# Kernel tuning notes

Measured on AMD Instinct MI355X. Metric: run time of the kernel, lower is better.

The kernel has to match this reference:

```python
import jax, jax.numpy as jnp
import numpy as np

NF = 64      # num_feat
NFR = 5      # num_frames
G = 8        # offset/deformable groups
CENTER = NFR // 2
K = 9        # 3x3 taps


def conv3x3(x, w, b):
    y = jax.lax.conv_general_dilated(x, w, (1, 1), 'SAME',
                                     dimension_numbers=('NCHW', 'OIHW', 'NCHW'))
    return y + b[None, :, None, None]


def mdcn(x, offsets, masks, w, b):
    # x: [B,C,H,W]; offsets: [B,2*G*K,H,W] (layout g,k,(y,x)); masks: [B,G*K,H,W]
    B, C, H, W = x.shape
    Cg = C // G
    off = offsets.reshape(B, G, K, 2, H, W)
    oy, ox = off[:, :, :, 0], off[:, :, :, 1]          # [B,G,K,H,W]
    m = masks.reshape(B, G, K, H, W)
    ky = jnp.repeat(jnp.arange(3), 3) - 1              # [K]
    kx = jnp.tile(jnp.arange(3), 3) - 1
    base_y = (ky[:, None, None] + jnp.arange(H)[None, :, None]).astype(x.dtype)  # [K,H,1]
    base_x = (kx[:, None, None] + jnp.arange(W)[None, None, :]).astype(x.dtype)  # [K,1,W]
    py = oy + base_y[None, None]                        # [B,G,K,H,W]
    px = ox + base_x[None, None]
    y0f = jnp.floor(py); x0f = jnp.floor(px)
    ty = py - y0f; tx = px - x0f
    y0 = y0f.astype(jnp.int32); x0 = x0f.astype(jnp.int32)
    xg = x.reshape(B, G, Cg, H * W)

    def gather(yi, xi):
        valid = (yi >= 0) & (yi < H) & (xi >= 0) & (xi < W)
        yc = jnp.clip(yi, 0, H - 1); xc = jnp.clip(xi, 0, W - 1)
        idx = (yc * W + xc).reshape(B, G, 1, K * H * W)
        idx = jnp.broadcast_to(idx, (B, G, Cg, K * H * W))
        v = jnp.take_along_axis(xg, idx, axis=3).reshape(B, G, Cg, K, H, W)
        return v * valid.reshape(B, G, 1, K, H, W)

    v00 = gather(y0, x0); v01 = gather(y0, x0 + 1)
    v10 = gather(y0 + 1, x0); v11 = gather(y0 + 1, x0 + 1)
    ty_ = ty[:, :, None]; tx_ = tx[:, :, None]          # [B,G,1,K,H,W]
    samp = (v00 * (1 - ty_) * (1 - tx_) + v01 * (1 - ty_) * tx_ +
            v10 * ty_ * (1 - tx_) + v11 * ty_ * tx_)
    samp = samp * m[:, :, None]                          # modulation
    wr = w.reshape(-1, G, Cg, K)                         # [Cout,G,Cg,K]
    out = jnp.einsum('bgckhw,ogck->bohw', samp, wr)
    return out + b[None, :, None, None]


def setup_inputs():
    key = jax.random.key(0)
    ks = jax.random.split(key, 16)
    def mk(k, shape, fan_in):
        return jax.random.normal(k, shape, jnp.float32) * (1.0 / np.sqrt(fan_in))
    B, H, W = 1, 160, 160
    return {
        'x':   jax.random.normal(ks[0], (B, NFR, 4, H, W), jnp.float32),
        'fw1': mk(ks[1], (NF, 4, 3, 3), 4 * 9),   'fb1': jnp.zeros((NF,), jnp.float32),
        'fw2': mk(ks[2], (NF, NF, 3, 3), NF * 9), 'fb2': jnp.zeros((NF,), jnp.float32),
        'fw3': mk(ks[3], (NF, NF, 3, 3), NF * 9), 'fb3': jnp.zeros((NF,), jnp.float32),
        'ow1': mk(ks[4], (NF, 2 * NF, 3, 3), 2 * NF * 9), 'ob1': jnp.zeros((NF,), jnp.float32),
        'ow2': mk(ks[5], (NF, NF, 3, 3), NF * 9),         'ob2': jnp.zeros((NF,), jnp.float32),
        'ow3': mk(ks[6], (G * 27, NF, 3, 3), NF * 9) * 0.1,
        'ob3': jnp.zeros((G * 27,), jnp.float32),
        'dw':  mk(ks[7], (NF, NF, 3, 3), NF * 9), 'db': jnp.zeros((NF,), jnp.float32),
    }


def reference(x, fw1, fb1, fw2, fb2, fw3, fb3, ow1, ob1, ow2, ob2, ow3, ob3, dw, db):
    B, N, C, H, W = x.shape
    f = x.reshape(B * N, C, H, W)
    f = jax.nn.relu(conv3x3(f, fw1, fb1))
    f = jax.nn.relu(conv3x3(f, fw2, fb2))
    f = jax.nn.relu(conv3x3(f, fw3, fb3))
    feats = f.reshape(B, N, NF, H, W)
    ref = feats[:, CENTER]                               # [B,NF,H,W]
    nc = np.array([i for i in range(N) if i != CENTER])
    curr = feats[:, nc].reshape(B * (N - 1), NF, H, W)
    ref_t = jnp.broadcast_to(ref[:, None], (B, N - 1, NF, H, W)).reshape(B * (N - 1), NF, H, W)
    cat = jnp.concatenate([ref_t, curr], axis=1)         # [B(N-1),2*NF,H,W]
    o = jax.nn.relu(conv3x3(cat, ow1, ob1))
    o = jax.nn.relu(conv3x3(o, ow2, ob2))
    raw = conv3x3(o, ow3, ob3)                           # [B(N-1),27G,H,W]
    offsets = raw[:, :G * 18]
    masks = jax.nn.sigmoid(raw[:, G * 18:])
    aligned = mdcn(curr, offsets, masks, dw, db)
    aligned = aligned.reshape(B, N - 1, NF, H, W)
    return jnp.concatenate([aligned[:, :CENTER], ref[:, None], aligned[:, CENTER:]], axis=1)
```

## Files before the change

### kernel.cpp

```cpp
#include <hip/hip_runtime.h>
#include <hip/hip_bf16.h>
#include <math.h>

#define HH 160
#define WW 160
#define HWsz (HH*WW)

typedef short bf16x8 __attribute__((ext_vector_type(8)));
typedef float f32x4  __attribute__((ext_vector_type(4)));

__device__ inline ushort f2bf(float f) {
    unsigned int u = __float_as_uint(f);
    unsigned int r = (u + 0x7FFFu + ((u >> 16) & 1u)) >> 16;
    return (ushort)r;
}

__device__ inline void unpk8(uint4 u, float* f) {
    f[0] = __uint_as_float(u.x << 16); f[1] = __uint_as_float(u.x & 0xFFFF0000u);
    f[2] = __uint_as_float(u.y << 16); f[3] = __uint_as_float(u.y & 0xFFFF0000u);
    f[4] = __uint_as_float(u.z << 16); f[5] = __uint_as_float(u.z & 0xFFFF0000u);
    f[6] = __uint_as_float(u.w << 16); f[7] = __uint_as_float(u.w & 0xFFFF0000u);
}

__global__ __launch_bounds__(256)
void pack_all(const float* __restrict__ fw2, const float* __restrict__ fw3,
              const float* __restrict__ ow1, const float* __restrict__ ow2,
              const float* __restrict__ ow3, const float* __restrict__ dw,
              ushort* __restrict__ w2p, ushort* __restrict__ w3p,
              ushort* __restrict__ o1p, ushort* __restrict__ o2p,
              ushort* __restrict__ o3p, ushort* __restrict__ wmp)
{
    const int seg = blockIdx.y;
    const int idx = blockIdx.x * 256 + threadIdx.x;

    if (seg == 5) {
        if (idx >= 18 * 4 * 64) return;
        const int lane = idx & 63;
        const int mt   = (idx >> 6) & 3;
        const int chunk = idx >> 8;
        const int o  = mt * 16 + (lane & 15);
        const int gk = chunk * 4 + (lane >> 4);
        const int g  = gk / 9, k = gk % 9;
        ushort v[8];
#pragma unroll
        for (int j = 0; j < 8; ++j)
            v[j] = f2bf(dw[((size_t)o * 64 + g * 8 + j) * 9 + k]);
        uint4 pk;
        pk.x = (unsigned)v[0] | ((unsigned)v[1] << 16);
        pk.y = (unsigned)v[2] | ((unsigned)v[3] << 16);
        pk.z = (unsigned)v[4] | ((unsigned)v[5] << 16);
        pk.w = (unsigned)v[6] | ((unsigned)v[7] << 16);
        *(uint4*)(wmp + (size_t)idx * 8) = pk;
        return;
    }

    const float* w; ushort* wp; int Cout, Cin, MT_TOT, CIC;
    switch (seg) {
        case 0: w = fw2; wp = w2p; Cout = 64;  Cin = 64;  MT_TOT = 4;  CIC = 2; break;
        case 1: w = fw3; wp = w3p; Cout = 64;  Cin = 64;  MT_TOT = 4;  CIC = 2; break;
        case 2: w = ow1; wp = o1p; Cout = 64;  Cin = 128; MT_TOT = 4;  CIC = 4; break;
        case 3: w = ow2; wp = o2p; Cout = 64;  Cin = 64;  MT_TOT = 4;  CIC = 2; break;
        default: w = ow3; wp = o3p; Cout = 216; Cin = 64; MT_TOT = 16; CIC = 2; break;
    }
    const int total = 9 * CIC * MT_TOT * 64;
    if (idx >= total) return;
    const int lane = idx & 63;
    int t = idx >> 6;
    const int mt  = t % MT_TOT; t /= MT_TOT;
    const int cic = t % CIC;    t /= CIC;
    const int tap = t;
    const int co  = mt * 16 + (lane & 15);
    const int ci0 = cic * 32 + (lane >> 4) * 8;
    ushort v[8];
#pragma unroll
    for (int j = 0; j < 8; ++j) {
        const int ci = ci0 + j;
        float f = 0.f;
        if (co < Cout && ci < Cin) f = w[((size_t)co * Cin + ci) * 9 + tap];
        v[j] = f2bf(f);
    }
    uint4 pk;
    pk.x = (unsigned)v[0] | ((unsigned)v[1] << 16);
    pk.y = (unsigned)v[2] | ((unsigned)v[3] << 16);
    pk.z = (unsigned)v[4] | ((unsigned)v[5] << 16);
    pk.w = (unsigned)v[6] | ((unsigned)v[7] << 16);
    *(uint4*)(wp + (size_t)idx * 8) = pk;
}

template<int CI_STEPS, bool CONCAT, bool RELU, int OMODE>
__global__ __launch_bounds__(256, 2)
void mfma_conv(const ushort* __restrict__ in, const ushort* __restrict__ wp,
               const float* __restrict__ bias, void* __restrict__ outv,
               int Cout, int MT_TOT, int COG,
               float* __restrict__ outmain, ushort* __restrict__ aux)
{
    constexpr int ROWS = 8, HR = ROWS + 2, NT = 4;
    constexpr int C8   = 8;
    constexpr int CICT = 2 * CI_STEPS;
    constexpr int CIN  = CICT * 32;
    __shared__ uint4 s_in4[HR * 34 * C8];
    __shared__ uint4 s_a4[9 * 4 * 64];

    const int tid = threadIdx.x;
    const int lane = tid & 63, wid = tid >> 6;
    const int lane15 = lane & 15, lgrp = lane >> 4;
    const int bz = blockIdx.z;
    const int frame = bz / COG, cog = bz % COG;
    const int x0 = blockIdx.x * 32, y0 = blockIdx.y * ROWS;

    const ushort* src = nullptr; const ushort* srcRef = nullptr; const ushort* srcCur = nullptr;
    if (CONCAT) {
        const int fidx = (frame < 2) ? frame : frame + 1;
        srcRef = in + (size_t)2 * HWsz * 64;
        srcCur = in + (size_t)fidx * HWsz * 64;
    } else {
        src = in + (size_t)frame * HWsz * CIN;
    }

    f32x4 acc[4][NT];
#pragma unroll
    for (int m = 0; m < 4; ++m)
#pragma unroll
        for (int n = 0; n < NT; ++n) acc[m][n] = (f32x4){0.f, 0.f, 0.f, 0.f};

    const uint4* wp4 = (const uint4*)wp;
    const int wrow = wid * 2;
    const int mtg0 = cog * 4;

#pragma unroll
    for (int step = 0; step < CI_STEPS; ++step) {
#pragma unroll
        for (int half = 0; half < 2; ++half) {
            if (half == 0) {
                for (int i = tid; i < HR * 34 * C8; i += 256) {
                    const int ci8l = i & (C8 - 1);
                    const int rem = i / C8;
                    const int col = rem % 34, row = rem / 34;
                    const int gy = y0 + row - 1, gx = x0 + col - 1;
                    const int gci8 = step * C8 + ci8l;
                    uint4 v = {0u, 0u, 0u, 0u};
                    if (gy >= 0 && gy < HH && gx >= 0 && gx < WW) {
                        if (CONCAT) {
                            const ushort* sp = (gci8 < 8) ? srcRef : srcCur;
                            v = *(const uint4*)(sp + (size_t)(gy * WW + gx) * 64 + (gci8 & 7) * 8);
                        } else {
                            v = *(const uint4*)(src + (size_t)(gy * WW + gx) * CIN + gci8 * 8);
                        }
                    }
                    s_in4[(row * 34 + col) * C8 + (ci8l ^ (col & 7))] = v;
                }
            }
#pragma unroll
            for (int it = 0; it < 9; ++it) {
                const int i = tid + it * 256;
                const int ln = i & 63, mt = (i >> 6) & 3, kkl = i >> 8;
                const int kkg = half * 9 + kkl;
                const int tap = kkg >> 1, cic = kkg & 1;
                s_a4[i] = wp4[((size_t)(tap * CICT + step * 2 + cic) * MT_TOT + mtg0 + mt) * 64 + ln];
            }
            __syncthreads();

#pragma unroll
            for (int kkl = 0; kkl < 9; ++kkl) {
                const int kkg = half * 9 + kkl;
                const int tap = kkg >> 1, cic = kkg & 1;
                const int dy  = tap / 3 - 1;
                const int dxp = tap % 3;
                bf16x8 a[4];
#pragma unroll
                for (int mt = 0; mt < 4; ++mt)
                    a[mt] = *(const bf16x8*)&s_a4[(kkl * 4 + mt) * 64 + lane];
#pragma unroll
                for (int nt = 0; nt < NT; ++nt) {
                    const int row_l = wrow + (nt >> 1) + dy + 1;
                    const int col_l = (nt & 1) * 16 + lane15 + dxp;
                    const bf16x8 b = *(const bf16x8*)
                        &s_in4[(row_l * 34 + col_l) * C8 + ((cic * 4 + lgrp) ^ (col_l & 7))];
#pragma unroll
                    for (int mt = 0; mt < 4; ++mt)
                        acc[mt][nt] = __builtin_amdgcn_mfma_f32_16x16x32_bf16(a[mt], b, acc[mt][nt], 0, 0, 0);
                }
            }
            __syncthreads();
        }
    }

#pragma unroll
    for (int mt = 0; mt < 4; ++mt) {
        const int co = cog * 64 + mt * 16 + lgrp * 4;
        if (co < Cout) {
            const float4 bs = *(const float4*)&bias[co];
#pragma unroll
            for (int nt = 0; nt < NT; ++nt) {
                const int yy = y0 + wrow + (nt >> 1);
                const int xx = x0 + (nt & 1) * 16 + lane15;
                const int hw = yy * WW + xx;
                f32x4 v = acc[mt][nt];
                v[0] += bs.x; v[1] += bs.y; v[2] += bs.z; v[3] += bs.w;
                if (RELU) {
                    v[0] = fmaxf(v[0], 0.f); v[1] = fmaxf(v[1], 0.f);
                    v[2] = fmaxf(v[2], 0.f); v[3] = fmaxf(v[3], 0.f);
                }
                if (OMODE <= 1) {
                    uint2 pk;
                    pk.x = (unsigned)f2bf(v[0]) | ((unsigned)f2bf(v[1]) << 16);
                    pk.y = (unsigned)f2bf(v[2]) | ((unsigned)f2bf(v[3]) << 16);
                    *(uint2*)((ushort*)outv + ((size_t)frame * HWsz + hw) * 64 + co) = pk;
                    if (OMODE == 1) {
                        if (frame == 2) {
#pragma unroll
                            for (int j = 0; j < 4; ++j)
                                outmain[((size_t)(128 + co + j)) * HWsz + hw] = v[j];
                        } else {
                            const int b = (frame < 2) ? frame : frame - 1;
                            *(uint2*)(aux + (((size_t)(b * 8 + (co >> 3)) * HWsz + hw) * 8 + (co & 7))) = pk;
                        }
                    }
                } else {
                    if (co < 144) {
                        const ushort h0 = f2bf(v[0]), h1 = f2bf(v[1]);
                        const ushort h2 = f2bf(v[2]), h3 = f2bf(v[3]);
                        unsigned* roff = (unsigned*)outv + (size_t)frame * 72 * HWsz;
                        roff[(size_t)(co >> 1) * HWsz + hw]       = (unsigned)h0 | ((unsigned)h1 << 16);
                        roff[(size_t)((co >> 1) + 1) * HWsz + hw] = (unsigned)h2 | ((unsigned)h3 << 16);
                    } else {
                        ushort* rmsk = aux + (size_t)frame * 72 * HWsz;
                        const int gk0 = co - 144;
#pragma unroll
                        for (int j = 0; j < 4; ++j) {
                            const float m = 1.f / (1.f + __expf(-v[j]));
                            rmsk[(size_t)(gk0 + j) * HWsz + hw] = f2bf(m);
                        }
                    }
                }
            }
        }
    }
}

__global__ __launch_bounds__(256)
void conv1_kernel(const float* __restrict__ x, const float* __restrict__ w,
                  const float* __restrict__ b, ushort* __restrict__ out)
{
    const int fr = blockIdx.z;
    const int t = threadIdx.x;
    const int tx = t & 15, ty = t >> 4;
    const int x0 = blockIdx.x * 16, y0 = blockIdx.y * 16;

    __shared__ float s_x[4][18][18];
    __shared__ float s_w[36][64];
    __shared__ float s_b[64];

    for (int i = t; i < 4 * 18 * 18; i += 256) {
        const int ci = i / 324, rem = i % 324;
        const int yy = rem / 18, xx = rem % 18;
        const int gy = y0 + yy - 1, gx = x0 + xx - 1;
        float v = 0.f;
        if (gy >= 0 && gy < HH && gx >= 0 && gx < WW)
            v = x[((size_t)fr * 4 + ci) * HWsz + gy * WW + gx];
        s_x[ci][yy][xx] = v;
    }
    for (int i = t; i < 36 * 64; i += 256) {
        const int row = i / 64, o = i % 64;
        const int ci = row / 9, tap = row % 9;
        s_w[row][o] = w[((size_t)o * 4 + ci) * 9 + tap];
    }
    if (t < 64) s_b[t] = b[t];
    __syncthreads();

    float acc[64];
#pragma unroll
    for (int i = 0; i < 64; ++i) acc[i] = 0.f;

#pragma unroll
    for (int ci = 0; ci < 4; ++ci) {
#pragma unroll
        for (int tap = 0; tap < 9; ++tap) {
            const float v = s_x[ci][ty + tap / 3][tx + tap % 3];
            const float4* wr = (const float4*)&s_w[ci * 9 + tap][0];
#pragma unroll
            for (int o4 = 0; o4 < 16; ++o4) {
                const float4 wv = wr[o4];
                acc[o4 * 4 + 0] = fmaf(v, wv.x, acc[o4 * 4 + 0]);
                acc[o4 * 4 + 1] = fmaf(v, wv.y, acc[o4 * 4 + 1]);
                acc[o4 * 4 + 2] = fmaf(v, wv.z, acc[o4 * 4 + 2]);
                acc[o4 * 4 + 3] = fmaf(v, wv.w, acc[o4 * 4 + 3]);
            }
        }
    }

    ushort* ob = out + ((size_t)fr * HWsz + (y0 + ty) * WW + (x0 + tx)) * 64;
#pragma unroll
    for (int o8 = 0; o8 < 8; ++o8) {
        ushort v[8];
#pragma unroll
        for (int j = 0; j < 8; ++j)
            v[j] = f2bf(fmaxf(acc[o8 * 8 + j] + s_b[o8 * 8 + j], 0.f));
        uint4 pk;
        pk.x = (unsigned)v[0] | ((unsigned)v[1] << 16);
        pk.y = (unsigned)v[2] | ((unsigned)v[3] << 16);
        pk.z = (unsigned)v[4] | ((unsigned)v[5] << 16);
        pk.w = (unsigned)v[6] | ((unsigned)v[7] << 16);
        *(uint4*)(ob + o8 * 8) = pk;
    }
}

__global__ __launch_bounds__(512, 4)
void mdcn_mfma(const ushort* __restrict__ ftsg, const unsigned* __restrict__ roffg,
               const ushort* __restrict__ rmskg,
               const ushort* __restrict__ wmp, const float* __restrict__ db,
               float* __restrict__ out)
{
    __shared__ uint4 s_w4[18 * 4 * 64];

    const int b    = blockIdx.z;
    const int fidx = (b < 2) ? b : b + 1;
    const int tid  = threadIdx.x;
    const int lane = tid & 63, wid = tid >> 6;
    const int lane15 = lane & 15, lgrp = lane >> 4;
    const int x = blockIdx.x * 16 + lane15;
    const int y = blockIdx.y * 8 + wid;
    const int hw = y * WW + x;

    const uint4* wmp4 = (const uint4*)wmp;
    for (int i = tid; i < 18 * 4 * 64; i += 512) s_w4[i] = wmp4[i];

    const unsigned* roff = roffg + (size_t)b * 72 * HWsz;
    const ushort*   rmsk = rmskg + (size_t)b * 72 * HWsz;

    unsigned opv[18];
#pragma unroll
    for (int n = 0; n < 18; ++n)
        opv[n] = roff[(size_t)(n * 4 + lgrp) * HWsz + hw];

    __syncthreads();

    f32x4 acc[4];
#pragma unroll
    for (int m = 0; m < 4; ++m) acc[m] = (f32x4){0.f, 0.f, 0.f, 0.f};

    auto prep = [&](int n, uint4& u00, uint4& u01, uint4& u10, uint4& u11,
                    float& w00, float& w01, float& w10, float& w11) {
        const int gk = n * 4 + lgrp;
        const int gg = gk / 9, k9 = gk - 9 * gg;
        const int kyy = k9 / 3 - 1, kxx = k9 - (k9 / 3) * 3 - 1;
        const unsigned op = opv[n];
        const float oy = __uint_as_float(op << 16);
        const float ox = __uint_as_float(op & 0xFFFF0000u);
        const float mv = __uint_as_float((unsigned)rmsk[(size_t)gk * HWsz + hw] << 16);

        const float py = oy + (float)(y + kyy);
        const float px = ox + (float)(x + kxx);
        const float y0f = floorf(py), x0f = floorf(px);
        const float tyf = py - y0f, txf = px - x0f;
        const int y0 = (int)y0f, x0i = (int)x0f;
        const int y1 = y0 + 1, x1 = x0i + 1;
        const bool vy0 = (y0 >= 0) & (y0 < HH);
        const bool vy1 = (y1 >= 0) & (y1 < HH);
        const bool vx0 = (x0i >= 0) & (x0i < WW);
        const bool vx1 = (x1 >= 0) & (x1 < WW);
        const int yc0 = min(max(y0, 0), HH - 1), yc1 = min(max(y1, 0), HH - 1);
        const int xc0 = min(max(x0i, 0), WW - 1), xc1 = min(max(x1, 0), WW - 1);
        const float a0 = (1.f - tyf) * mv, a1 = tyf * mv;
        w00 = a0 * (1.f - txf);
        w01 = a0 * txf;
        w10 = a1 * (1.f - txf);
        w11 = a1 * txf;
        if (!(vy0 && vx0)) w00 = 0.f;
        if (!(vy0 && vx1)) w01 = 0.f;
        if (!(vy1 && vx0)) w10 = 0.f;
        if (!(vy1 && vx1)) w11 = 0.f;

        const ushort* pb = ftsg + (size_t)(b * 8 + gg) * HWsz * 8;
        u00 = *(const uint4*)(pb + (size_t)(yc0 * WW + xc0) * 8);
        u01 = *(const uint4*)(pb + (size_t)(yc0 * WW + xc1) * 8);
        u10 = *(const uint4*)(pb + (size_t)(yc1 * WW + xc0) * 8);
        u11 = *(const uint4*)(pb + (size_t)(yc1 * WW + xc1) * 8);
    };

    uint4 cu00, cu01, cu10, cu11;
    float cw00, cw01, cw10, cw11;
    prep(0, cu00, cu01, cu10, cu11, cw00, cw01, cw10, cw11);

#pragma unroll
    for (int g = 0; g < 18; ++g) {
        uint4 nu00, nu01, nu10, nu11;
        float nw00, nw01, nw10, nw11;
        if (g < 17)
            prep(g + 1, nu00, nu01, nu10, nu11, nw00, nw01, nw10, nw11);

        float f00[8], f01[8], f10[8], f11[8];
        unpk8(cu00, f00); unpk8(cu01, f01); unpk8(cu10, f10); unpk8(cu11, f11);
        float s[8];
#pragma unroll
        for (int c = 0; c < 8; ++c)
            s[c] = fmaf(cw11, f11[c], fmaf(cw10, f10[c],
                    fmaf(cw01, f01[c], cw00 * f00[c])));
        uint4 bpk;
        asm("v_cvt_pk_bf16_f32 %0, %1, %2" : "=v"(bpk.x) : "v"(s[0]), "v"(s[1]));
        asm("v_cvt_pk_bf16_f32 %0, %1, %2" : "=v"(bpk.y) : "v"(s[2]), "v"(s[3]));
        asm("v_cvt_pk_bf16_f32 %0, %1, %2" : "=v"(bpk.z) : "v"(s[4]), "v"(s[5]));
        asm("v_cvt_pk_bf16_f32 %0, %1, %2" : "=v"(bpk.w) : "v"(s[6]), "v"(s[7]));
        const bf16x8 bfrag = __builtin_bit_cast(bf16x8, bpk);

#pragma unroll
        for (int mt = 0; mt < 4; ++mt) {
            const bf16x8 a = *(const bf16x8*)&s_w4[(g * 4 + mt) * 64 + lane];
            acc[mt] = __builtin_amdgcn_mfma_f32_16x16x32_bf16(a, bfrag, acc[mt], 0, 0, 0);
        }

        if (g < 17) {
            cu00 = nu00; cu01 = nu01; cu10 = nu10; cu11 = nu11;
            cw00 = nw00; cw01 = nw01; cw10 = nw10; cw11 = nw11;
        }
    }

    float* ob = out + (size_t)fidx * 64 * HWsz + hw;
#pragma unroll
    for (int mt = 0; mt < 4; ++mt) {
        const int o0 = mt * 16 + lgrp * 4;
        const float4 bs = *(const float4*)&db[o0];
        ob[(size_t)(o0 + 0) * HWsz] = acc[mt][0] + bs.x;
        ob[(size_t)(o0 + 1) * HWsz] = acc[mt][1] + bs.y;
        ob[(size_t)(o0 + 2) * HWsz] = acc[mt][2] + bs.z;
        ob[(size_t)(o0 + 3) * HWsz] = acc[mt][3] + bs.w;
    }
}

extern "C" void kernel_launch(void* const* d_in, const int* in_sizes, int n_in,
                              void* d_out, int out_size, void* d_ws, size_t ws_size,
                              hipStream_t stream)
{
    const float* x   = (const float*)d_in[0];
    const float* fw1 = (const float*)d_in[1];
    const float* fb1 = (const float*)d_in[2];
    const float* fw2 = (const float*)d_in[3];
    const float* fb2 = (const float*)d_in[4];
    const float* fw3 = (const float*)d_in[5];
    const float* fb3 = (const float*)d_in[6];
    const float* ow1 = (const float*)d_in[7];
    const float* ob1 = (const float*)d_in[8];
    const float* ow2 = (const float*)d_in[9];
    const float* ob2 = (const float*)d_in[10];
    const float* ow3 = (const float*)d_in[11];
    const float* ob3 = (const float*)d_in[12];
    const float* dw  = (const float*)d_in[13];
    const float* db  = (const float*)d_in[14];
    float* out = (float*)d_out;

    ushort* buf1 = (ushort*)d_ws;
    ushort* buf2 = buf1 + (size_t)5 * HWsz * 64;
    ushort* fts  = buf2 + (size_t)5 * HWsz * 64;
    ushort* ftsg = fts + (size_t)5 * HWsz * 64;
    unsigned* roff = (unsigned*)(ftsg + (size_t)4 * 8 * HWsz * 8);
    ushort* rmsk = (ushort*)(roff + (size_t)4 * 72 * HWsz);
    ushort* w2p  = rmsk + (size_t)4 * 72 * HWsz;
    ushort* w3p  = w2p + 36864;
    ushort* o1p  = w3p + 36864;
    ushort* o2p  = o1p + 73728;
    ushort* o3p  = o2p + 36864;
    ushort* wmp  = o3p + 147456;

    const dim3 blk(256);

    pack_all<<<dim3(72, 6), blk, 0, stream>>>(fw2, fw3, ow1, ow2, ow3, dw,
                                              w2p, w3p, o1p, o2p, o3p, wmp);

    conv1_kernel<<<dim3(10, 10, 5), blk, 0, stream>>>(x, fw1, fb1, buf1);
    mfma_conv<1, false, true, 0><<<dim3(5, 20, 5), blk, 0, stream>>>(
        buf1, w2p, fb2, buf2, 64, 4, 1, nullptr, nullptr);
    mfma_conv<1, false, true, 1><<<dim3(5, 20, 5), blk, 0, stream>>>(
        buf2, w3p, fb3, fts, 64, 4, 1, out, ftsg);

    mfma_conv<2, true, true, 0><<<dim3(5, 20, 4), blk, 0, stream>>>(
        fts, o1p, ob1, buf1, 64, 4, 1, nullptr, nullptr);
    mfma_conv<1, false, true, 0><<<dim3(5, 20, 4), blk, 0, stream>>>(
        buf1, o2p, ob2, buf2, 64, 4, 1, nullptr, nullptr);
    mfma_conv<1, false, false, 3><<<dim3(5, 20, 16), blk, 0, stream>>>(
        buf2, o3p, ob3, roff, 216, 16, 4, nullptr, rmsk);

    mdcn_mfma<<<dim3(10, 20, 4), dim3(512), 0, stream>>>(ftsg, roff, rmsk, wmp, db, out);
}
```

Baseline: 205.3 us.

## Add dedicated offset-conv kernel computing 128 output channels per block

Replaces the generic mfma_conv launch for the final offset/mask conv (216 outputs, split into 4 channel groups of 64) with a specialized kernel where each block computes 8 M-tiles (128 channels), halving the channel groups to 2. The input halo tile is loaded to shared memory once per block and reused across twice as many output channels. Weight fragments for the next k-step are prefetched into registers. The intent is to cut redundant input staging and raise MFMA density per shared-memory load, at the cost of higher register pressure (launch bounds 256,2) and some wasted compute on the padded second group (256 vs 216 channels).

```diff
diff --git a/kernel.cpp b/kernel.cpp
--- a/kernel.cpp
+++ b/kernel.cpp
@@ -201,36 +201,124 @@
                     v[0] = fmaxf(v[0], 0.f); v[1] = fmaxf(v[1], 0.f);
                     v[2] = fmaxf(v[2], 0.f); v[3] = fmaxf(v[3], 0.f);
                 }
-                if (OMODE <= 1) {
-                    uint2 pk;
-                    pk.x = (unsigned)f2bf(v[0]) | ((unsigned)f2bf(v[1]) << 16);
-                    pk.y = (unsigned)f2bf(v[2]) | ((unsigned)f2bf(v[3]) << 16);
-                    *(uint2*)((ushort*)outv + ((size_t)frame * HWsz + hw) * 64 + co) = pk;
-                    if (OMODE == 1) {
-                        if (frame == 2) {
-#pragma unroll
-                            for (int j = 0; j < 4; ++j)
-                                outmain[((size_t)(128 + co + j)) * HWsz + hw] = v[j];
-                        } else {
-                            const int b = (frame < 2) ? frame : frame - 1;
-                            *(uint2*)(aux + (((size_t)(b * 8 + (co >> 3)) * HWsz + hw) * 8 + (co & 7))) = pk;
-                        }
+                uint2 pk;
+                pk.x = (unsigned)f2bf(v[0]) | ((unsigned)f2bf(v[1]) << 16);
+                pk.y = (unsigned)f2bf(v[2]) | ((unsigned)f2bf(v[3]) << 16);
+                *(uint2*)((ushort*)outv + ((size_t)frame * HWsz + hw) * 64 + co) = pk;
+                if (OMODE == 1) {
+                    if (frame == 2) {
+#pragma unroll
+                        for (int j = 0; j < 4; ++j)
+                            outmain[((size_t)(128 + co + j)) * HWsz + hw] = v[j];
+                    } else {
+                        const int b = (frame < 2) ? frame : frame - 1;
+                        *(uint2*)(aux + (((size_t)(b * 8 + (co >> 3)) * HWsz + hw) * 8 + (co & 7))) = pk;
                     }
+                }
+            }
+        }
+    }
+}
+
+__global__ __launch_bounds__(256, 2)
+void mfma_conv_ow3(const ushort* __restrict__ in, const ushort* __restrict__ wp,
+                   const float* __restrict__ bias,
+                   unsigned* __restrict__ roffg, ushort* __restrict__ rmskg)
+{
+    constexpr int HR = 10, C8 = 8, NT = 4, MT = 8;
+    __shared__ uint4 s_in4[HR * 34 * C8];
+
+    const int tid = threadIdx.x;
+    const int lane = tid & 63, wid = tid >> 6;
+    const int lane15 = lane & 15, lgrp = lane >> 4;
+    const int bz = blockIdx.z;
+    const int frame = bz >> 1, cog = bz & 1;
+    const int x0 = blockIdx.x * 32, y0 = blockIdx.y * 8;
+
+    const ushort* src = in + (size_t)frame * HWsz * 64;
+    const uint4* wp4 = (const uint4*)wp;
+    const int wrow = wid * 2;
+    const int mtg0 = cog * 8;
+
+    f32x4 acc[MT][NT];
+#pragma unroll
+    for (int m = 0; m < MT; ++m)
+#pragma unroll
+        for (int n = 0; n < NT; ++n) acc[m][n] = (f32x4){0.f, 0.f, 0.f, 0.f};
+
+    uint4 a_cur[MT], a_nxt[MT];
+#pragma unroll
+    for (int mt = 0; mt < MT; ++mt)
+        a_cur[mt] = wp4[((size_t)0 * 16 + mtg0 + mt) * 64 + lane];
+
+    for (int i = tid; i < HR * 34 * C8; i += 256) {
+        const int ci8l = i & (C8 - 1);
+        const int rem = i / C8;
+        const int col = rem % 34, row = rem / 34;
+        const int gy = y0 + row - 1, gx = x0 + col - 1;
+        uint4 v = {0u, 0u, 0u, 0u};
+        if (gy >= 0 && gy < HH && gx >= 0 && gx < WW)
+            v = *(const uint4*)(src + (size_t)(gy * WW + gx) * 64 + ci8l * 8);
+        s_in4[(row * 34 + col) * C8 + (ci8l ^ (col & 7))] = v;
+    }
+    __syncthreads();
+
+#pragma unroll
+    for (int kk = 0; kk < 18; ++kk) {
+        if (kk < 17) {
+#pragma unroll
+            for (int mt = 0; mt < MT; ++mt)
+                a_nxt[mt] = wp4[((size_t)(kk + 1) * 16 + mtg0 + mt) * 64 + lane];
+        }
+        const int tap = kk >> 1, cic = kk & 1;
+        const int dy  = tap / 3 - 1;
+        const int dxp = tap % 3;
+#pragma unroll
+        for (int nt = 0; nt < NT; ++nt) {
+            const int row_l = wrow + (nt >> 1) + dy + 1;
+            const int col_l = (nt & 1) * 16 + lane15 + dxp;
+            const bf16x8 b = *(const bf16x8*)
+                &s_in4[(row_l * 34 + col_l) * C8 + ((cic * 4 + lgrp) ^ (col_l & 7))];
+#pragma unroll
+            for (int mt = 0; mt < MT; ++mt)
+                acc[mt][nt] = __builtin_amdgcn_mfma_f32_16x16x32_bf16(
+                    *(const bf16x8*)&a_cur[mt], b, acc[mt][nt], 0, 0, 0);
+        }
+        if (kk < 17) {
+#pragma unroll
+            for (int mt = 0; mt < MT; ++mt)
+                asm volatile("" : "+v"(a_nxt[mt].x), "+v"(a_nxt[mt].y),
+                                  "+v"(a_nxt[mt].z), "+v"(a_nxt[mt].w));
+#pragma unroll
+            for (int mt = 0; mt < MT; ++mt) a_cur[mt] = a_nxt[mt];
+        }
+    }
+
+    unsigned* roff = roffg + (size_t)frame * 72 * HWsz;
+    ushort*   rmsk = rmskg + (size_t)frame * 72 * HWsz;
+#pragma unroll
+    for (int mt = 0; mt < MT; ++mt) {
+        const int co = cog * 128 + mt * 16 + lgrp * 4;
+        if (co < 216) {
+            const float4 bs = *(const float4*)&bias[co];
+#pragma unroll
+            for (int nt = 0; nt < NT; ++nt) {
+                const int yy = y0 + wrow + (nt >> 1);
+                const int xx = x0 + (nt & 1) * 16 + lane15;
+                const int hw = yy * WW + xx;
+                f32x4 v = acc[mt][nt];
+                v[0] += bs.x; v[1] += bs.y; v[2] += bs.z; v[3] += bs.w;
+                if (co < 144) {
+                    const ushort h0 = f2bf(v[0]), h1 = f2bf(v[1]);
+                    const ushort h2 = f2bf(v[2]), h3 = f2bf(v[3]);
+                    roff[(size_t)(co >> 1) * HWsz + hw]       = (unsigned)h0 | ((unsigned)h1 << 16);
+                    roff[(size_t)((co >> 1) + 1) * HWsz + hw] = (unsigned)h2 | ((unsigned)h3 << 16);
                 } else {
-                    if (co < 144) {
-                        const ushort h0 = f2bf(v[0]), h1 = f2bf(v[1]);
-                        const ushort h2 = f2bf(v[2]), h3 = f2bf(v[3]);
-                        unsigned* roff = (unsigned*)outv + (size_t)frame * 72 * HWsz;
-                        roff[(size_t)(co >> 1) * HWsz + hw]       = (unsigned)h0 | ((unsigned)h1 << 16);
-                        roff[(size_t)((co >> 1) + 1) * HWsz + hw] = (unsigned)h2 | ((unsigned)h3 << 16);
-                    } else {
-                        ushort* rmsk = aux + (size_t)frame * 72 * HWsz;
-                        const int gk0 = co - 144;
-#pragma unroll
-                        for (int j = 0; j < 4; ++j) {
-                            const float m = 1.f / (1.f + __expf(-v[j]));
-                            rmsk[(size_t)(gk0 + j) * HWsz + hw] = f2bf(m);
-                        }
+                    const int gk0 = co - 144;
+#pragma unroll
+                    for (int j = 0; j < 4; ++j) {
+                        const float m = 1.f / (1.f + __expf(-v[j]));
+                        rmsk[(size_t)(gk0 + j) * HWsz + hw] = f2bf(m);
                     }
                 }
             }
@@ -476,8 +564,7 @@
         fts, o1p, ob1, buf1, 64, 4, 1, nullptr, nullptr);
     mfma_conv<1, false, true, 0><<<dim3(5, 20, 4), blk, 0, stream>>>(
         buf1, o2p, ob2, buf2, 64, 4, 1, nullptr, nullptr);
-    mfma_conv<1, false, false, 3><<<dim3(5, 20, 16), blk, 0, stream>>>(
-        buf2, o3p, ob3, roff, 216, 16, 4, nullptr, rmsk);
+    mfma_conv_ow3<<<dim3(5, 20, 8), blk, 0, stream>>>(buf2, o3p, ob3, roff, rmsk);
 
     mdcn_mfma<<<dim3(10, 20, 4), dim3(512), 0, stream>>>(ftsg, roff, rmsk, wmp, db, out);
 }
```

New measurement: 214.5 us. 1.04x slower.
